# Kernel optimization log

Hardware: AMD Instinct MI355X
Metric: run time of the kernel (lower is better)

The kernel has to match this reference:

```python
import jax, jax.numpy as jnp
import numpy as np
import math

B, LAT, HID, T, NCLS = 128, 128, 256, 1920, 3
EPS = 1e-5


def _ln(x, g, b):
    m = jnp.mean(x, axis=-1, keepdims=True)
    v = jnp.var(x, axis=-1, keepdims=True)
    return (x - m) * jax.lax.rsqrt(v + EPS) * g + b


def _leaky(x):
    return jax.nn.leaky_relu(x, 0.2)


def _lstm_layer(x, Wih, Whh, bih, bhh):
    # x: [T, B, D] time-major; gate order i,f,g,o (PyTorch convention)
    xw = jnp.einsum('tbd,gd->tbg', x, Wih) + bih + bhh  # precompute input projection
    Hd = Whh.shape[1]
    bsz = x.shape[1]

    def step(carry, xg):
        h, c = carry
        gates = xg + h @ Whh.T
        i, f, g, o = jnp.split(gates, 4, axis=-1)
        c = jax.nn.sigmoid(f) * c + jax.nn.sigmoid(i) * jnp.tanh(g)
        h = jax.nn.sigmoid(o) * jnp.tanh(c)
        return (h, c), h

    init = (jnp.zeros((bsz, Hd), x.dtype), jnp.zeros((bsz, Hd), x.dtype))
    _, hs = jax.lax.scan(step, init, xw)
    return hs  # [T, B, H]


def setup_inputs() -> dict:
    key = jax.random.key(0)
    ks = jax.random.split(key, 16)
    s = 0.05
    H2 = HID // 2
    d = {
        'z': jax.random.normal(ks[0], (B, LAT), jnp.float32),
        'labels': jax.random.randint(ks[1], (B,), 0, 4, jnp.int64),
        'emb_W': jax.random.normal(ks[2], (NCLS + 1, HID), jnp.float32) * s,
        'np_W': jax.random.normal(ks[3], (HID, LAT + HID), jnp.float32) * s,
        'np_b': jnp.zeros((HID,), jnp.float32),
        'np_g': jnp.ones((HID,), jnp.float32),
        'np_be': jnp.zeros((HID,), jnp.float32),
        'Wih0': jax.random.normal(ks[4], (4 * HID, 2 * HID), jnp.float32) * s,
        'Whh0': jax.random.normal(ks[5], (4 * HID, HID), jnp.float32) * s,
        'bih0': jnp.zeros((4 * HID,), jnp.float32),
        'bhh0': jnp.zeros((4 * HID,), jnp.float32),
        'Wih1': jax.random.normal(ks[6], (4 * HID, HID), jnp.float32) * s,
        'Whh1': jax.random.normal(ks[7], (4 * HID, HID), jnp.float32) * s,
        'bih1': jnp.zeros((4 * HID,), jnp.float32),
        'bhh1': jnp.zeros((4 * HID,), jnp.float32),
        'oW1': jax.random.normal(ks[8], (H2, HID), jnp.float32) * s,
        'ob1': jnp.zeros((H2,), jnp.float32),
        'og': jnp.ones((H2,), jnp.float32),
        'obe': jnp.zeros((H2,), jnp.float32),
        'oW2': jax.random.normal(ks[9], (3, H2), jnp.float32) * s,
        'ob2': jnp.zeros((3,), jnp.float32),
        'sW1': jax.random.normal(ks[10], (H2, HID), jnp.float32) * s,
        'sb1': jnp.zeros((H2,), jnp.float32),
        'sg': jnp.ones((H2,), jnp.float32),
        'sbe': jnp.zeros((H2,), jnp.float32),
        'sW2': jax.random.normal(ks[11], (1, H2), jnp.float32) * s,
        'sb2': jnp.zeros((1,), jnp.float32),
        'stress_w': jnp.array(1.8, jnp.float32),
        'amu_w': jnp.array([0.15, 0.7, 0.15], jnp.float32),
        'amu_b': jnp.array(-0.3, jnp.float32),
    }
    return d


def reference(z, labels, emb_W, np_W, np_b, np_g, np_be, Wih0, Whh0, bih0, bhh0,
              Wih1, Whh1, bih1, bhh1, oW1, ob1, og, obe, oW2, ob2,
              sW1, sb1, sg, sbe, sW2, sb2, stress_w, amu_w, amu_b):
    bsz = z.shape[0]
    emb = emb_W[labels]                                   # [B, H]
    h = _leaky(_ln(jnp.concatenate([z, emb], axis=1) @ np_W.T + np_b, np_g, np_be))
    # [B, T, 2H]
    sig_in = jnp.concatenate([
        jnp.broadcast_to(h[:, None, :], (bsz, T, HID)),
        jnp.broadcast_to(emb[:, None, :], (bsz, T, HID)),
    ], axis=2)
    x = jnp.transpose(sig_in, (1, 0, 2))                  # time-major [T, B, 2H]
    x = _lstm_layer(x, Wih0, Whh0, bih0, bhh0)
    x = _lstm_layer(x, Wih1, Whh1, bih1, bhh1)
    ch = jnp.transpose(x, (1, 0, 2))                      # [B, T, H]

    # oscillation params per sample (vectorized over batch)
    h_avg = jnp.mean(ch, axis=1)                          # [B, H]
    op = _leaky(_ln(h_avg @ oW1.T + ob1, og, obe)) @ oW2.T + ob2  # [B, 3]
    freq = 0.23 + 0.04 * jnp.tanh(op[:, 0])
    amp = 2.0 + 1.5 * jnp.tanh(op[:, 1])
    phase = math.pi * jax.nn.sigmoid(op[:, 2])
    t = jnp.linspace(0.0, 1.0, T)
    osc = amp[:, None] * jnp.sin(2.0 * math.pi * freq[:, None] * T * t[None, :] + phase[:, None])  # [B, T]

    base = jnp.tanh(_leaky(_ln(ch @ sW1.T + sb1, sg, sbe)) @ sW2.T + sb2)  # [B, T, 1]
    enhanced = 0.6 * base[..., 0] + 0.4 * osc             # [B, T]

    stressed = stress_w * enhanced                        # conv1d k=1, w=1.8
    xp = jnp.pad(enhanced, ((0, 0), (1, 1)))
    smoothed = amu_w[0] * xp[:, :-2] + amu_w[1] * xp[:, 1:-1] + amu_w[2] * xp[:, 2:] + amu_b

    lab = labels[:, None]
    out = jnp.where(lab == 1, enhanced,
          jnp.where(lab == 2, stressed,
          jnp.where(lab == 3, smoothed, jnp.zeros_like(enhanced))))
    return out[..., None]                                  # [B, T, 1]
```

## Files before the change

### kernel.cpp

```cpp
#include <hip/hip_runtime.h>

#define TSTEPS 1920
#define NB 128
#define HIDN 256
#define LATN 128
#define EPSF 1e-5f

typedef __attribute__((ext_vector_type(8))) short bf16x8;
typedef __attribute__((ext_vector_type(4))) float f32x4;

__device__ __forceinline__ unsigned short f2bf(float x) {
    unsigned u = __builtin_bit_cast(unsigned, x);
    unsigned r = (u + 0x7fffu + ((u >> 16) & 1u)) >> 16;
    return (unsigned short)r;
}
__device__ __forceinline__ float bf2f(unsigned short h) {
    unsigned u = ((unsigned)h) << 16;
    return __builtin_bit_cast(float, u);
}
__device__ __forceinline__ float fsig(float x) {
    float e = __expf(-fabsf(x));
    float s = 1.f / (1.f + e);
    return x >= 0.f ? s : 1.f - s;
}
__device__ __forceinline__ float ftanh(float x) {
    float e = __expf(-2.f * fabsf(x));
    float r = (1.f - e) / (1.f + e);
    return x >= 0.f ? r : -r;
}
__device__ __forceinline__ float fleaky(float x) { return x > 0.f ? x : 0.2f * x; }
__device__ __forceinline__ bf16x8 bcast16(uint4 v) { return __builtin_bit_cast(bf16x8, v); }

__device__ __forceinline__ unsigned aload(const unsigned* p) {
    return __hip_atomic_load(p, __ATOMIC_RELAXED, __HIP_MEMORY_SCOPE_AGENT);
}
__device__ __forceinline__ unsigned long long aload64(const unsigned long long* p) {
    return __hip_atomic_load(p, __ATOMIC_RELAXED, __HIP_MEMORY_SCOPE_AGENT);
}
__device__ __forceinline__ void astore(unsigned* p, unsigned v) {
    __hip_atomic_store(p, v, __ATOMIC_RELAXED, __HIP_MEMORY_SCOPE_AGENT);
}

#define MFMA(a, b, c) __builtin_amdgcn_mfma_f32_16x16x32_bf16((a), (b), (c), 0, 0, 0)

#define FLG(g, s) ((g) * 8 + (s)) * 32
#define HPLANE(g, layer, buf) (((g) * 2 + (layer)) * 2 + (buf)) * 4096

__global__ void init_sync(unsigned* hbuf, unsigned* flags) {
    int i = blockIdx.x * 256 + threadIdx.x;
    if (i < 131072) hbuf[i] = 0u;
    if (i < 4096) flags[i] = 0u;
}

__global__ void pack_bfrag_sliced(const float* __restrict__ A, const float* __restrict__ Bsrc,
                                  int KA, int KB,
                                  unsigned short* __restrict__ hi, unsigned short* __restrict__ lo) {
    int e = blockIdx.x * 256 + threadIdx.x;
    int K = KA + KB;
    int KT = K >> 5;
    if (e >= 1024 * K) return;
    int j = e & 7;
    int l = (e >> 3) & 63;
    int r = e >> 9;
    int kt = r % KT;
    int r2 = r / KT;
    int v = r2 & 7;
    int w = r2 >> 3;
    int n = (v >> 1) * 256 + 32 * w + 16 * (v & 1) + (l & 15);
    int k = kt * 32 + (l >> 4) * 8 + j;
    float val = (k < KA) ? A[n * KA + k] : Bsrc[n * KB + (k - KA)];
    unsigned short h = f2bf(val);
    hi[e] = h;
    lo[e] = f2bf(val - bf2f(h));
}

__global__ void pack_sw1frag(const float* __restrict__ sW1, unsigned short* __restrict__ out) {
    int e = blockIdx.x * 256 + threadIdx.x;
    if (e >= 32768) return;
    int j3 = e & 7;
    int l = (e >> 3) & 63;
    int r = e >> 9;
    int kt = r & 7, w = r >> 3;
    int n = w * 16 + (l & 15);
    int k = kt * 32 + (l >> 4) * 8 + j3;
    out[e] = f2bf(sW1[n * 256 + k]);
}

__global__ void pack4T(const float* __restrict__ W, int N, int K, float* __restrict__ out) {
    int e = blockIdx.x * 256 + threadIdx.x;
    if (e >= N * K) return;
    int j = e & 3;
    int rest = e >> 2;
    int n = rest % N;
    int k4 = rest / N;
    out[e] = W[n * K + 4 * k4 + j];
}

__global__ void prep_b1(const float* __restrict__ bih1, const float* __restrict__ bhh1,
                        float* __restrict__ b1sum) {
    int i = blockIdx.x * 256 + threadIdx.x;
    if (i < 1024) b1sum[i] = bih1[i] + bhh1[i];
}

__global__ void np_head(const float* __restrict__ z, const int* __restrict__ labels,
                        const float* __restrict__ emb_W, const float* __restrict__ np_W,
                        const float* __restrict__ np_b, const float* __restrict__ np_g,
                        const float* __restrict__ np_be, float* __restrict__ x_const) {
    int b = blockIdx.x;
    int j = threadIdx.x;
    __shared__ float xc[LATN + HIDN];
    __shared__ float red[8];
    int lab = labels[b];
    if (j < LATN) xc[j] = z[b * LATN + j];
    float e = emb_W[lab * HIDN + j];
    xc[LATN + j] = e;
    __syncthreads();
    float d = np_b[j];
    for (int k = 0; k < LATN + HIDN; ++k) d += xc[k] * np_W[j * (LATN + HIDN) + k];
    int lane = j & 63, wv = j >> 6;
    float s = d, s2 = d * d;
    for (int o = 1; o < 64; o <<= 1) { s += __shfl_xor(s, o); s2 += __shfl_xor(s2, o); }
    if (lane == 0) { red[wv] = s; red[4 + wv] = s2; }
    __syncthreads();
    float S = red[0] + red[1] + red[2] + red[3];
    float S2 = red[4] + red[5] + red[6] + red[7];
    float m = S * (1.f / 256.f);
    float var = S2 * (1.f / 256.f) - m * m;
    float h = fleaky((d - m) * rsqrtf(var + EPSF) * np_g[j] + np_be[j]);
    x_const[b * 512 + j] = h;
    x_const[b * 512 + 256 + j] = e;
}

__global__ void __launch_bounds__(1024) xw0_kernel(const float* __restrict__ x_const,
                                                   const float4* __restrict__ Wih0T4,
                                                   const float* __restrict__ bih0,
                                                   const float* __restrict__ bhh0,
                                                   float* __restrict__ xw0) {
    int b = blockIdx.x;
    int g = threadIdx.x;
    __shared__ float xc[512];
    if (g < 512) xc[g] = x_const[b * 512 + g];
    __syncthreads();
    const float4* xc4 = (const float4*)xc;
    float4 acc = {0.f, 0.f, 0.f, 0.f};
#pragma unroll 8
    for (int k4 = 0; k4 < 128; ++k4) {
        float4 w = Wih0T4[k4 * 1024 + g];
        float4 x = xc4[k4];
        acc.x = fmaf(w.x, x.x, acc.x);
        acc.y = fmaf(w.y, x.y, acc.y);
        acc.z = fmaf(w.z, x.z, acc.z);
        acc.w = fmaf(w.w, x.w, acc.w);
    }
    xw0[b * 1024 + g] = bih0[g] + bhh0[g] + ((acc.x + acc.y) + (acc.z + acc.w));
}

__global__ void __launch_bounds__(512, 2) lstm_coop(
    const uint4* __restrict__ whh0h, const uint4* __restrict__ whh0l,
    const uint4* __restrict__ w1h, const uint4* __restrict__ w1l,
    const unsigned short* __restrict__ sw1f_g, const float* __restrict__ xw0g,
    const float* __restrict__ b1sum, const float* __restrict__ sb1,
    const float* __restrict__ sg, const float* __restrict__ sbe,
    const float* __restrict__ sW2, const float* __restrict__ sb2,
    unsigned* __restrict__ hbuf, unsigned* __restrict__ flags,
    float* __restrict__ base_out, float* __restrict__ hsum_out) {
    extern __shared__ char smem[];
    char* pHhi = smem;
    char* pHlo = smem + 16384;
    unsigned short* sw1f = (unsigned short*)(smem + 32768);
    float* gates0 = (float*)(smem + 98304);
    float* gates1 = (float*)(smem + 106752);
    float* s1b = (float*)(smem + 115200);

    const int gidx = blockIdx.x & 7;
    const int W = blockIdx.x >> 3;
    const int g16 = gidx * 16;
    const int tid = threadIdx.x;
    const int l = tid & 63;
    const int v = tid >> 6;
    const int ln16 = l & 15;
    const int kg = l >> 4;

    for (int i = tid; i < 16384; i += 512)
        ((unsigned*)sw1f)[i] = ((const unsigned*)sw1f_g)[i];

    uint4 b0h[8], b0l[8];
#pragma unroll
    for (int kt = 0; kt < 8; ++kt) {
        int idx = ((W * 8 + v) * 8 + kt) * 64 + l;
        b0h[kt] = whh0h[idx];
        b0l[kt] = whh0l[idx];
    }
    uint4 w1hR[16], w1lR[16];
#pragma unroll
    for (int kt = 0; kt < 16; ++kt) {
        int idx = ((W * 8 + v) * 16 + kt) * 64 + l;
        w1hR[kt] = w1h[idx];
        w1lR[kt] = w1l[idx];
    }

    const int row = tid >> 5;
    const int ul = tid & 31;
    const int ug = 32 * W + ul;
    float xwi[4], b1v[4];
#pragma unroll
    for (int gt = 0; gt < 4; ++gt) {
        xwi[gt] = xw0g[(g16 + row) * 1024 + gt * 256 + ug];
        b1v[gt] = b1sum[gt * 256 + ug];
    }
    float c0 = 0.f, c1 = 0.f, hs = 0.f;

    const float sb1a = sb1[2 * l], sb1b = sb1[2 * l + 1];
    const float sga = sg[2 * l], sgb = sg[2 * l + 1];
    const float sbea = sbe[2 * l], sbeb = sbe[2 * l + 1];
    const float sw2a = sW2[2 * l], sw2b = sW2[2 * l + 1];
    const float sb2v = sb2[0];

    unsigned* h0buf[2] = {hbuf + HPLANE(gidx, 0, 0), hbuf + HPLANE(gidx, 0, 1)};
    unsigned* h1buf[2] = {hbuf + HPLANE(gidx, 1, 0), hbuf + HPLANE(gidx, 1, 1)};
    unsigned* fl = flags + FLG(gidx, W);
    unsigned* flbase = flags + FLG(gidx, 0);

    const int abase = ln16 * 1024;
    const int aswz = (ln16 & 7) << 4;
    const int kgo = kg * 16;
    const int gcol = (v >> 1) * 32 + (v & 1) * 16 + ln16;

#define WAITF(tgtv)                                                              \
    {                                                                            \
        unsigned tgt = (unsigned)(tgtv);                                         \
        while (true) {                                                           \
            unsigned val = (l < 8) ? aload(flbase + l * 32) : tgt;               \
            if (__all((int)(val >= tgt))) break;                                 \
            __builtin_amdgcn_s_sleep(1);                                         \
        }                                                                        \
    }                                                                            \
    asm volatile("" ::: "memory");

#define STAGE2(src0, src1)                                                       \
    {                                                                            \
        const unsigned long long* sA = (const unsigned long long*)(src0);        \
        const unsigned long long* sB = (const unsigned long long*)(src1);        \
        _Pragma("unroll")                                                        \
        for (int it = 0; it < 4; ++it) {                                         \
            int i2 = tid + 512 * it;                                             \
            int r_ = i2 >> 7, u2 = i2 & 127;                                     \
            int swz = (r_ & 7) << 4;                                             \
            int off0 = r_ * 1024 + ((4 * u2) ^ swz);                             \
            unsigned long long vA = aload64(sA + r_ * 128 + u2);                 \
            unsigned a0 = (unsigned)vA, a1 = (unsigned)(vA >> 32);               \
            *(unsigned*)(pHhi + off0) = (a0 >> 16) | (a1 & 0xffff0000u);         \
            *(unsigned*)(pHlo + off0) = (a0 & 0xffffu) | (a1 << 16);             \
            int off1 = r_ * 1024 + ((512 + 4 * u2) ^ swz);                       \
            unsigned long long vB = aload64(sB + r_ * 128 + u2);                 \
            unsigned e0 = (unsigned)vB, e1 = (unsigned)(vB >> 32);               \
            *(unsigned*)(pHhi + off1) = (e0 >> 16) | (e1 & 0xffff0000u);         \
            *(unsigned*)(pHlo + off1) = (e0 & 0xffffu) | (e1 << 16);             \
        }                                                                        \
    }

#define HEADFIN(tout)                                                            \
    if (v < 4) {                                                                 \
        _Pragma("unroll")                                                        \
        for (int r4 = 0; r4 < 4; ++r4) {                                         \
            int hrw = v * 4 + r4;                                                \
            float2 sv = *(const float2*)&s1b[hrw * 132 + 2 * l];                 \
            float sA = sv.x + sb1a, sB = sv.y + sb1b;                            \
            float ssum = sA + sB, ssq = sA * sA + sB * sB;                       \
            _Pragma("unroll")                                                    \
            for (int o = 1; o < 64; o <<= 1) {                                   \
                ssum += __shfl_xor(ssum, o); ssq += __shfl_xor(ssq, o);          \
            }                                                                    \
            float m = ssum * (1.f / 128.f);                                      \
            float var = ssq * (1.f / 128.f) - m * m;                             \
            float rstd = rsqrtf(var + EPSF);                                     \
            float p0 = fleaky((sA - m) * rstd * sga + sbea);                     \
            float p1 = fleaky((sB - m) * rstd * sgb + sbeb);                     \
            float qd = p0 * sw2a + p1 * sw2b;                                    \
            _Pragma("unroll")                                                    \
            for (int o = 1; o < 64; o <<= 1) qd += __shfl_xor(qd, o);            \
            if (l == 0) base_out[(g16 + hrw) * TSTEPS + (tout)] = ftanh(qd + sb2v); \
        }                                                                        \
    }

    __syncthreads();

    for (int p = 0; p <= TSTEPS; ++p) {
        WAITF(p);
        STAGE2(h0buf[(p - 1) & 1], h1buf[p & 1]);
        __syncthreads();
        {
            f32x4 a0 = {0.f, 0.f, 0.f, 0.f};
            f32x4 a1 = {0.f, 0.f, 0.f, 0.f};
            f32x4 ah = {0.f, 0.f, 0.f, 0.f};
#pragma unroll
            for (int kt = 0; kt < 8; ++kt) {
                int aoff = abase + ((kt * 64 + kgo) ^ aswz);
                bf16x8 ahi = bcast16(*(const uint4*)(pHhi + aoff));
                bf16x8 alo = bcast16(*(const uint4*)(pHlo + aoff));
                bf16x8 bh = bcast16(b0h[kt]);
                bf16x8 bl = bcast16(b0l[kt]);
                a0 = MFMA(ahi, bh, a0); a0 = MFMA(alo, bh, a0); a0 = MFMA(ahi, bl, a0);
                bf16x8 ch = bcast16(w1hR[kt]);
                bf16x8 cl = bcast16(w1lR[kt]);
                a1 = MFMA(ahi, ch, a1); a1 = MFMA(alo, ch, a1); a1 = MFMA(ahi, cl, a1);
            }
#pragma unroll
            for (int kt = 8; kt < 16; ++kt) {
                int aoff = abase + ((kt * 64 + kgo) ^ aswz);
                bf16x8 ahi = bcast16(*(const uint4*)(pHhi + aoff));
                bf16x8 alo = bcast16(*(const uint4*)(pHlo + aoff));
                bf16x8 ch = bcast16(w1hR[kt]);
                bf16x8 cl = bcast16(w1lR[kt]);
                a1 = MFMA(ahi, ch, a1); a1 = MFMA(alo, ch, a1); a1 = MFMA(ahi, cl, a1);
                bf16x8 bsw = bcast16(*(const uint4*)&sw1f[((v * 8 + (kt - 8)) * 64 + l) * 8]);
                ah = MFMA(ahi, bsw, ah); ah = MFMA(alo, bsw, ah);
            }
#pragma unroll
            for (int r = 0; r < 4; ++r) {
                gates0[(kg * 4 + r) * 132 + gcol] = a0[r];
                gates1[(kg * 4 + r) * 132 + gcol] = a1[r];
                s1b[(kg * 4 + r) * 132 + v * 16 + ln16] = ah[r];
            }
        }
        __syncthreads();
        {
            float i_ = gates0[row * 132 + ul] + xwi[0];
            float f_ = gates0[row * 132 + 32 + ul] + xwi[1];
            float g_ = gates0[row * 132 + 64 + ul] + xwi[2];
            float o_ = gates0[row * 132 + 96 + ul] + xwi[3];
            c0 = fsig(f_) * c0 + fsig(i_) * ftanh(g_);
            float h = fsig(o_) * ftanh(c0);
            unsigned short hh = f2bf(h);
            unsigned short ll = f2bf(h - bf2f(hh));
            astore(h0buf[p & 1] + row * 256 + ug, ((unsigned)hh << 16) | (unsigned)ll);
        }
        if (p > 0) {
            float i_ = gates1[row * 132 + ul] + b1v[0];
            float f_ = gates1[row * 132 + 32 + ul] + b1v[1];
            float g_ = gates1[row * 132 + 64 + ul] + b1v[2];
            float o_ = gates1[row * 132 + 96 + ul] + b1v[3];
            c1 = fsig(f_) * c1 + fsig(i_) * ftanh(g_);
            float h = fsig(o_) * ftanh(c1);
            hs += h;
            unsigned short hh = f2bf(h);
            unsigned short ll = f2bf(h - bf2f(hh));
            astore(h1buf[(p - 1) & 1] + row * 256 + ug, ((unsigned)hh << 16) | (unsigned)ll);
        }
        asm volatile("s_waitcnt vmcnt(0)" ::: "memory");
        __syncthreads();
        if (tid == 0) astore(fl, (unsigned)(p + 1));
        if (p >= 2) HEADFIN(p - 2);
    }
    WAITF(TSTEPS + 1);
    STAGE2(h0buf[(TSTEPS + 1 - 1) & 1], h1buf[(TSTEPS + 1) & 1]);
    __syncthreads();
    {
        f32x4 ah = {0.f, 0.f, 0.f, 0.f};
#pragma unroll
        for (int kt = 8; kt < 16; ++kt) {
            int aoff = abase + ((kt * 64 + kgo) ^ aswz);
            bf16x8 ahi = bcast16(*(const uint4*)(pHhi + aoff));
            bf16x8 alo = bcast16(*(const uint4*)(pHlo + aoff));
            bf16x8 bsw = bcast16(*(const uint4*)&sw1f[((v * 8 + (kt - 8)) * 64 + l) * 8]);
            ah = MFMA(ahi, bsw, ah); ah = MFMA(alo, bsw, ah);
        }
#pragma unroll
        for (int r = 0; r < 4; ++r) s1b[(kg * 4 + r) * 132 + v * 16 + ln16] = ah[r];
    }
    __syncthreads();
    HEADFIN(TSTEPS - 1);
    hsum_out[(g16 + row) * HIDN + ug] = hs;
#undef WAITF
#undef STAGE2
#undef HEADFIN
}

__global__ void out_kernel(const float* __restrict__ hsum, const float* __restrict__ oW1,
                           const float* __restrict__ ob1, const float* __restrict__ og,
                           const float* __restrict__ obe, const float* __restrict__ oW2,
                           const float* __restrict__ ob2, const float* __restrict__ base,
                           const int* __restrict__ labels, const float* __restrict__ stress_w,
                           const float* __restrict__ amu_w, const float* __restrict__ amu_b,
                           float* __restrict__ out) {
    int b = blockIdx.x;
    int tid = threadIdx.x;
    int lane = tid & 63, wv = tid >> 6;
    __shared__ float havg[256];
    __shared__ float red[8];
    __shared__ float params[3];
    __shared__ float e_row[TSTEPS];
    havg[tid] = hsum[b * 256 + tid] * (1.f / (float)TSTEPS);
    __syncthreads();
    float d1 = 0.f;
    if (tid < 128) {
        d1 = ob1[tid];
        for (int k = 0; k < 256; ++k) d1 += havg[k] * oW1[tid * 256 + k];
    }
    float s = d1, s2 = d1 * d1;
    for (int o = 1; o < 64; o <<= 1) { s += __shfl_xor(s, o); s2 += __shfl_xor(s2, o); }
    if (lane == 0 && wv < 2) { red[wv] = s; red[2 + wv] = s2; }
    __syncthreads();
    float m = (red[0] + red[1]) * (1.f / 128.f);
    float var = (red[2] + red[3]) * (1.f / 128.f) - m * m;
    float rstd = rsqrtf(var + EPSF);
    float p = 0.f;
    if (tid < 128) p = fleaky((d1 - m) * rstd * og[tid] + obe[tid]);
    float q0 = tid < 128 ? p * oW2[0 * 128 + tid] : 0.f;
    float q1 = tid < 128 ? p * oW2[1 * 128 + tid] : 0.f;
    float q2 = tid < 128 ? p * oW2[2 * 128 + tid] : 0.f;
    for (int o = 1; o < 64; o <<= 1) {
        q0 += __shfl_xor(q0, o); q1 += __shfl_xor(q1, o); q2 += __shfl_xor(q2, o);
    }
    __syncthreads();
    if (lane == 0 && wv < 2) { red[wv] = q0; red[2 + wv] = q1; red[4 + wv] = q2; }
    __syncthreads();
    if (tid == 0) {
        float op0 = red[0] + red[1] + ob2[0];
        float op1 = red[2] + red[3] + ob2[1];
        float op2 = red[4] + red[5] + ob2[2];
        params[0] = 0.23f + 0.04f * ftanh(op0);
        params[1] = 2.0f + 1.5f * ftanh(op1);
        params[2] = 3.14159265358979f * fsig(op2);
    }
    __syncthreads();
    float freq = params[0], amp = params[1], ph = params[2];
    for (int t = tid; t < TSTEPS; t += 256) {
        float x = freq * ((float)TSTEPS * (float)t / (float)(TSTEPS - 1));
        x -= floorf(x);
        float osc = amp * __sinf(6.28318530717958647f * x + ph);
        e_row[t] = 0.6f * base[b * TSTEPS + t] + 0.4f * osc;
    }
    __syncthreads();
    int lab = labels[b];
    float sw = stress_w[0];
    float w0 = amu_w[0], w1 = amu_w[1], w2 = amu_w[2], ab = amu_b[0];
    for (int t = tid; t < TSTEPS; t += 256) {
        float e = e_row[t];
        float r;
        if (lab == 1) r = e;
        else if (lab == 2) r = sw * e;
        else if (lab == 3) {
            float em = t > 0 ? e_row[t - 1] : 0.f;
            float ep = t < TSTEPS - 1 ? e_row[t + 1] : 0.f;
            r = w0 * em + w1 * e + w2 * ep + ab;
        } else r = 0.f;
        out[b * TSTEPS + t] = r;
    }
}

extern "C" void kernel_launch(void* const* d_in, const int* in_sizes, int n_in,
                              void* d_out, int out_size, void* d_ws, size_t ws_size,
                              hipStream_t stream) {
    (void)in_sizes; (void)n_in; (void)out_size; (void)ws_size;
    const float* z      = (const float*)d_in[0];
    const int* labels   = (const int*)d_in[1];
    const float* emb_W  = (const float*)d_in[2];
    const float* np_W   = (const float*)d_in[3];
    const float* np_b   = (const float*)d_in[4];
    const float* np_g   = (const float*)d_in[5];
    const float* np_be  = (const float*)d_in[6];
    const float* Wih0   = (const float*)d_in[7];
    const float* Whh0   = (const float*)d_in[8];
    const float* bih0   = (const float*)d_in[9];
    const float* bhh0   = (const float*)d_in[10];
    const float* Wih1   = (const float*)d_in[11];
    const float* Whh1   = (const float*)d_in[12];
    const float* bih1   = (const float*)d_in[13];
    const float* bhh1   = (const float*)d_in[14];
    const float* oW1    = (const float*)d_in[15];
    const float* ob1    = (const float*)d_in[16];
    const float* og     = (const float*)d_in[17];
    const float* obe    = (const float*)d_in[18];
    const float* oW2    = (const float*)d_in[19];
    const float* ob2    = (const float*)d_in[20];
    const float* sW1    = (const float*)d_in[21];
    const float* sb1    = (const float*)d_in[22];
    const float* sg     = (const float*)d_in[23];
    const float* sbe    = (const float*)d_in[24];
    const float* sW2    = (const float*)d_in[25];
    const float* sb2    = (const float*)d_in[26];
    const float* stressw= (const float*)d_in[27];
    const float* amu_w  = (const float*)d_in[28];
    const float* amu_b  = (const float*)d_in[29];
    float* out = (float*)d_out;

    uint8_t* ws = (uint8_t*)d_ws;
    size_t off = 0;
    unsigned short* whh0h = (unsigned short*)(ws + off); off += (size_t)1024 * 256 * 2;
    unsigned short* whh0l = (unsigned short*)(ws + off); off += (size_t)1024 * 256 * 2;
    unsigned short* w1h   = (unsigned short*)(ws + off); off += (size_t)1024 * 512 * 2;
    unsigned short* w1l   = (unsigned short*)(ws + off); off += (size_t)1024 * 512 * 2;
    unsigned short* sw1fg = (unsigned short*)(ws + off); off += (size_t)32768 * 2;
    float* Wih0T4 = (float*)(ws + off); off += (size_t)1024 * 512 * 4;
    float* x_const= (float*)(ws + off); off += (size_t)NB * 512 * 4;
    float* xw0    = (float*)(ws + off); off += (size_t)NB * 1024 * 4;
    float* b1sum  = (float*)(ws + off); off += (size_t)1024 * 4;
    float* hsum   = (float*)(ws + off); off += (size_t)NB * 256 * 4;
    float* basef  = (float*)(ws + off); off += (size_t)NB * TSTEPS * 4;
    off = (off + 255) & ~(size_t)255;
    unsigned* hbuf = (unsigned*)(ws + off); off += (size_t)131072 * 4;
    unsigned* flags= (unsigned*)(ws + off); off += (size_t)4096 * 4;

    init_sync<<<512, 256, 0, stream>>>(hbuf, flags);
    pack_bfrag_sliced<<<1024, 256, 0, stream>>>(Whh0, nullptr, 256, 0, whh0h, whh0l);
    pack_bfrag_sliced<<<2048, 256, 0, stream>>>(Wih1, Whh1, 256, 256, w1h, w1l);
    pack_sw1frag<<<128, 256, 0, stream>>>(sW1, sw1fg);
    pack4T<<<2048, 256, 0, stream>>>(Wih0, 1024, 512, Wih0T4);
    prep_b1<<<4, 256, 0, stream>>>(bih1, bhh1, b1sum);

    np_head<<<NB, 256, 0, stream>>>(z, labels, emb_W, np_W, np_b, np_g, np_be, x_const);
    xw0_kernel<<<NB, 1024, 0, stream>>>(x_const, (const float4*)Wih0T4, bih0, bhh0, xw0);
    lstm_coop<<<64, 512, 123648, stream>>>((const uint4*)whh0h, (const uint4*)whh0l,
                                           (const uint4*)w1h, (const uint4*)w1l,
                                           sw1fg, xw0, b1sum, sb1, sg, sbe, sW2, sb2,
                                           hbuf, flags, basef, hsum);
    out_kernel<<<NB, 256, 0, stream>>>(hsum, oW1, ob1, og, obe, oW2, ob2, basef, labels,
                                       stressw, amu_w, amu_b, out);
}
```

Baseline: 27.60 ms.

## Split each batch group into two half-groups with interleaved independent recurrence phases

Each workgroup's 16-row batch slice is split into two independent 8-row sub-groups, each with its own h buffers, flags and LDS staging planes. Every timestep now runs two sub-phases back to back, so the cross-workgroup flag wait of one sub-group can overlap the compute of the other. The cost is twice as many wait/sync rounds per step, MFMAs that now carry only half the rows, more LDS (156KB), and more register pressure.

```diff
diff --git a/kernel.cpp b/kernel.cpp
--- a/kernel.cpp
+++ b/kernel.cpp
@@ -44,7 +44,7 @@
 #define MFMA(a, b, c) __builtin_amdgcn_mfma_f32_16x16x32_bf16((a), (b), (c), 0, 0, 0)
 
 #define FLG(g, s) ((g) * 8 + (s)) * 32
-#define HPLANE(g, layer, buf) (((g) * 2 + (layer)) * 2 + (buf)) * 4096
+#define HPLANE(g, layer, buf) ((((g) * 2 + (layer)) * 2 + (buf)) * 2048)
 
 __global__ void init_sync(unsigned* hbuf, unsigned* flags) {
     int i = blockIdx.x * 256 + threadIdx.x;
@@ -165,16 +165,17 @@
     unsigned* __restrict__ hbuf, unsigned* __restrict__ flags,
     float* __restrict__ base_out, float* __restrict__ hsum_out) {
     extern __shared__ char smem[];
-    char* pHhi = smem;
-    char* pHlo = smem + 16384;
-    unsigned short* sw1f = (unsigned short*)(smem + 32768);
-    float* gates0 = (float*)(smem + 98304);
-    float* gates1 = (float*)(smem + 106752);
-    float* s1b = (float*)(smem + 115200);
-
-    const int gidx = blockIdx.x & 7;
+    char* pAhi = smem;
+    char* pAlo = smem + 16384;
+    char* pBhi = smem + 32768;
+    char* pBlo = smem + 49152;
+    unsigned short* sw1f = (unsigned short*)(smem + 65536);
+    float* gates0 = (float*)(smem + 131072);
+    float* gates1 = (float*)(smem + 139520);
+    float* s1b    = (float*)(smem + 147968);
+
+    const int g8 = blockIdx.x & 7;
     const int W = blockIdx.x >> 3;
-    const int g16 = gidx * 16;
     const int tid = threadIdx.x;
     const int l = tid & 63;
     const int v = tid >> 6;
@@ -183,6 +184,10 @@
 
     for (int i = tid; i < 16384; i += 512)
         ((unsigned*)sw1f)[i] = ((const unsigned*)sw1f_g)[i];
+    for (int i = tid; i < 4096; i += 512) {
+        ((unsigned*)pAhi)[i] = 0u; ((unsigned*)pAlo)[i] = 0u;
+        ((unsigned*)pBhi)[i] = 0u; ((unsigned*)pBlo)[i] = 0u;
+    }
 
     uint4 b0h[8], b0l[8];
 #pragma unroll
@@ -199,16 +204,18 @@
         w1lR[kt] = w1l[idx];
     }
 
-    const int row = tid >> 5;
+    const int r8 = (tid >> 5) & 7;
     const int ul = tid & 31;
     const int ug = 32 * W + ul;
-    float xwi[4], b1v[4];
+    float xwiA[4], xwiB[4], b1v[4];
 #pragma unroll
     for (int gt = 0; gt < 4; ++gt) {
-        xwi[gt] = xw0g[(g16 + row) * 1024 + gt * 256 + ug];
+        xwiA[gt] = xw0g[(16 * g8 + r8) * 1024 + gt * 256 + ug];
+        xwiB[gt] = xw0g[(16 * g8 + 8 + r8) * 1024 + gt * 256 + ug];
         b1v[gt] = b1sum[gt * 256 + ug];
     }
-    float c0 = 0.f, c1 = 0.f, hs = 0.f;
+    float c0A = 0.f, c1A = 0.f, hsA = 0.f;
+    float c0B = 0.f, c1B = 0.f, hsB = 0.f;
 
     const float sb1a = sb1[2 * l], sb1b = sb1[2 * l + 1];
     const float sga = sg[2 * l], sgb = sg[2 * l + 1];
@@ -216,51 +223,128 @@
     const float sw2a = sW2[2 * l], sw2b = sW2[2 * l + 1];
     const float sb2v = sb2[0];
 
-    unsigned* h0buf[2] = {hbuf + HPLANE(gidx, 0, 0), hbuf + HPLANE(gidx, 0, 1)};
-    unsigned* h1buf[2] = {hbuf + HPLANE(gidx, 1, 0), hbuf + HPLANE(gidx, 1, 1)};
-    unsigned* fl = flags + FLG(gidx, W);
-    unsigned* flbase = flags + FLG(gidx, 0);
+    unsigned* h0A[2] = {hbuf + HPLANE(2 * g8, 0, 0), hbuf + HPLANE(2 * g8, 0, 1)};
+    unsigned* h1A[2] = {hbuf + HPLANE(2 * g8, 1, 0), hbuf + HPLANE(2 * g8, 1, 1)};
+    unsigned* h0B[2] = {hbuf + HPLANE(2 * g8 + 1, 0, 0), hbuf + HPLANE(2 * g8 + 1, 0, 1)};
+    unsigned* h1B[2] = {hbuf + HPLANE(2 * g8 + 1, 1, 0), hbuf + HPLANE(2 * g8 + 1, 1, 1)};
+    unsigned* flA = flags + FLG(2 * g8, W);
+    unsigned* flAb = flags + FLG(2 * g8, 0);
+    unsigned* flB = flags + FLG(2 * g8 + 1, W);
+    unsigned* flBb = flags + FLG(2 * g8 + 1, 0);
 
     const int abase = ln16 * 1024;
     const int aswz = (ln16 & 7) << 4;
     const int kgo = kg * 16;
     const int gcol = (v >> 1) * 32 + (v & 1) * 16 + ln16;
 
-#define WAITF(tgtv)                                                              \
+#define WAITF(BASE, tgtv)                                                        \
     {                                                                            \
         unsigned tgt = (unsigned)(tgtv);                                         \
         while (true) {                                                           \
-            unsigned val = (l < 8) ? aload(flbase + l * 32) : tgt;               \
+            unsigned val = (l < 8) ? aload((BASE) + l * 32) : tgt;               \
             if (__all((int)(val >= tgt))) break;                                 \
             __builtin_amdgcn_s_sleep(1);                                         \
         }                                                                        \
     }                                                                            \
     asm volatile("" ::: "memory");
 
-#define STAGE2(src0, src1)                                                       \
+#define STAGE2(DH, DL, SRC0, SRC1)                                               \
     {                                                                            \
-        const unsigned long long* sA = (const unsigned long long*)(src0);        \
-        const unsigned long long* sB = (const unsigned long long*)(src1);        \
+        const unsigned long long* sA_ = (const unsigned long long*)(SRC0);       \
+        const unsigned long long* sB_ = (const unsigned long long*)(SRC1);       \
         _Pragma("unroll")                                                        \
         for (int it = 0; it < 4; ++it) {                                         \
             int i2 = tid + 512 * it;                                             \
-            int r_ = i2 >> 7, u2 = i2 & 127;                                     \
-            int swz = (r_ & 7) << 4;                                             \
-            int off0 = r_ * 1024 + ((4 * u2) ^ swz);                             \
-            unsigned long long vA = aload64(sA + r_ * 128 + u2);                 \
-            unsigned a0 = (unsigned)vA, a1 = (unsigned)(vA >> 32);               \
-            *(unsigned*)(pHhi + off0) = (a0 >> 16) | (a1 & 0xffff0000u);         \
-            *(unsigned*)(pHlo + off0) = (a0 & 0xffffu) | (a1 << 16);             \
-            int off1 = r_ * 1024 + ((512 + 4 * u2) ^ swz);                       \
-            unsigned long long vB = aload64(sB + r_ * 128 + u2);                 \
-            unsigned e0 = (unsigned)vB, e1 = (unsigned)(vB >> 32);               \
-            *(unsigned*)(pHhi + off1) = (e0 >> 16) | (e1 & 0xffff0000u);         \
-            *(unsigned*)(pHlo + off1) = (e0 & 0xffffu) | (e1 << 16);             \
-        }                                                                        \
-    }
-
-#define HEADFIN(tout)                                                            \
-    if (v < 4) {                                                                 \
+            int rr = i2 >> 7, u2 = i2 & 127;                                     \
+            int prow = rr & 7;                                                   \
+            int bas = (rr >> 3) * 512;                                           \
+            const unsigned long long* sp = (rr < 8) ? sA_ : sB_;                 \
+            unsigned long long vv = aload64(sp + prow * 128 + u2);               \
+            unsigned w0_ = (unsigned)vv, w1_ = (unsigned)(vv >> 32);             \
+            int off = prow * 1024 + ((bas + 4 * u2) ^ (prow << 4));              \
+            *(unsigned*)((DH) + off) = (w0_ >> 16) | (w1_ & 0xffff0000u);        \
+            *(unsigned*)((DL) + off) = (w0_ & 0xffffu) | (w1_ << 16);            \
+        }                                                                        \
+    }
+
+#define MVPHASE(PH, PL)                                                          \
+    {                                                                            \
+        f32x4 a0 = {0.f, 0.f, 0.f, 0.f};                                         \
+        f32x4 a1 = {0.f, 0.f, 0.f, 0.f};                                         \
+        f32x4 ahd = {0.f, 0.f, 0.f, 0.f};                                        \
+        _Pragma("unroll")                                                        \
+        for (int kt = 0; kt < 8; ++kt) {                                         \
+            int aoff = abase + ((kt * 64 + kgo) ^ aswz);                         \
+            bf16x8 ahi = bcast16(*(const uint4*)((PH) + aoff));                  \
+            bf16x8 alo = bcast16(*(const uint4*)((PL) + aoff));                  \
+            bf16x8 bh = bcast16(b0h[kt]);                                        \
+            bf16x8 bl = bcast16(b0l[kt]);                                        \
+            a0 = MFMA(ahi, bh, a0); a0 = MFMA(alo, bh, a0); a0 = MFMA(ahi, bl, a0); \
+            bf16x8 ch = bcast16(w1hR[kt]);                                       \
+            bf16x8 cl = bcast16(w1lR[kt]);                                       \
+            a1 = MFMA(ahi, ch, a1); a1 = MFMA(alo, ch, a1); a1 = MFMA(ahi, cl, a1); \
+        }                                                                        \
+        _Pragma("unroll")                                                        \
+        for (int kt = 8; kt < 16; ++kt) {                                        \
+            int aoff = abase + ((kt * 64 + kgo) ^ aswz);                         \
+            bf16x8 ahi = bcast16(*(const uint4*)((PH) + aoff));                  \
+            bf16x8 alo = bcast16(*(const uint4*)((PL) + aoff));                  \
+            bf16x8 ch = bcast16(w1hR[kt]);                                       \
+            bf16x8 cl = bcast16(w1lR[kt]);                                       \
+            a1 = MFMA(ahi, ch, a1); a1 = MFMA(alo, ch, a1); a1 = MFMA(ahi, cl, a1); \
+            bf16x8 bsw = bcast16(*(const uint4*)&sw1f[((v * 8 + (kt - 8)) * 64 + l) * 8]); \
+            ahd = MFMA(ahi, bsw, ahd); ahd = MFMA(alo, bsw, ahd);                \
+        }                                                                        \
+        _Pragma("unroll")                                                        \
+        for (int r = 0; r < 4; ++r) {                                            \
+            gates0[(kg * 4 + r) * 132 + gcol] = a0[r];                           \
+            gates1[(kg * 4 + r) * 132 + gcol] = a1[r];                           \
+            s1b[(kg * 4 + r) * 132 + v * 16 + ln16] = ahd[r];                    \
+        }                                                                        \
+    }
+
+#define HEADMV(PH, PL)                                                           \
+    {                                                                            \
+        f32x4 ahd = {0.f, 0.f, 0.f, 0.f};                                        \
+        _Pragma("unroll")                                                        \
+        for (int kt = 8; kt < 16; ++kt) {                                        \
+            int aoff = abase + ((kt * 64 + kgo) ^ aswz);                         \
+            bf16x8 ahi = bcast16(*(const uint4*)((PH) + aoff));                  \
+            bf16x8 alo = bcast16(*(const uint4*)((PL) + aoff));                  \
+            bf16x8 bsw = bcast16(*(const uint4*)&sw1f[((v * 8 + (kt - 8)) * 64 + l) * 8]); \
+            ahd = MFMA(ahi, bsw, ahd); ahd = MFMA(alo, bsw, ahd);                \
+        }                                                                        \
+        _Pragma("unroll")                                                        \
+        for (int r = 0; r < 4; ++r) s1b[(kg * 4 + r) * 132 + v * 16 + ln16] = ahd[r]; \
+    }
+
+#define UPDPUB(pp, H0B, H1B, XWI, C0, C1, HS)                                    \
+    if (tid < 256) {                                                             \
+        float i_ = gates0[r8 * 132 + ul] + (XWI)[0];                             \
+        float f_ = gates0[r8 * 132 + 32 + ul] + (XWI)[1];                        \
+        float g_ = gates0[r8 * 132 + 64 + ul] + (XWI)[2];                        \
+        float o_ = gates0[r8 * 132 + 96 + ul] + (XWI)[3];                        \
+        C0 = fsig(f_) * C0 + fsig(i_) * ftanh(g_);                               \
+        float h = fsig(o_) * ftanh(C0);                                          \
+        unsigned short hh = f2bf(h);                                             \
+        unsigned short ll = f2bf(h - bf2f(hh));                                  \
+        astore((H0B)[(pp) & 1] + r8 * 256 + ug, ((unsigned)hh << 16) | (unsigned)ll); \
+        if ((pp) > 0) {                                                          \
+            i_ = gates1[r8 * 132 + ul] + b1v[0];                                 \
+            f_ = gates1[r8 * 132 + 32 + ul] + b1v[1];                            \
+            g_ = gates1[r8 * 132 + 64 + ul] + b1v[2];                            \
+            o_ = gates1[r8 * 132 + 96 + ul] + b1v[3];                            \
+            C1 = fsig(f_) * C1 + fsig(i_) * ftanh(g_);                           \
+            h = fsig(o_) * ftanh(C1);                                            \
+            HS += h;                                                             \
+            hh = f2bf(h);                                                        \
+            ll = f2bf(h - bf2f(hh));                                             \
+            astore((H1B)[((pp) - 1) & 1] + r8 * 256 + ug, ((unsigned)hh << 16) | (unsigned)ll); \
+        }                                                                        \
+    }
+
+#define HEADFIN(GROW, tout)                                                      \
+    if (v < 2) {                                                                 \
         _Pragma("unroll")                                                        \
         for (int r4 = 0; r4 < 4; ++r4) {                                         \
             int hrw = v * 4 + r4;                                                \
@@ -279,101 +363,53 @@
             float qd = p0 * sw2a + p1 * sw2b;                                    \
             _Pragma("unroll")                                                    \
             for (int o = 1; o < 64; o <<= 1) qd += __shfl_xor(qd, o);            \
-            if (l == 0) base_out[(g16 + hrw) * TSTEPS + (tout)] = ftanh(qd + sb2v); \
-        }                                                                        \
-    }
+            if (l == 0) base_out[((GROW) + hrw) * TSTEPS + (tout)] = ftanh(qd + sb2v); \
+        }                                                                        \
+    }
+
+#define SUBPHASE(pp, PH, PL, H0B, H1B, FLW, FLWB, XWI, C0, C1, HS, GROW)         \
+    WAITF(FLWB, pp);                                                             \
+    STAGE2(PH, PL, (H0B)[((pp) - 1) & 1], (H1B)[(pp) & 1]);                      \
+    __syncthreads();                                                             \
+    MVPHASE(PH, PL);                                                             \
+    __syncthreads();                                                             \
+    UPDPUB(pp, H0B, H1B, XWI, C0, C1, HS);                                       \
+    asm volatile("s_waitcnt vmcnt(0)" ::: "memory");                             \
+    __syncthreads();                                                             \
+    if (tid == 0) astore(FLW, (unsigned)((pp) + 1));                             \
+    if ((pp) >= 2) HEADFIN(GROW, (pp) - 2);
 
     __syncthreads();
 
     for (int p = 0; p <= TSTEPS; ++p) {
-        WAITF(p);
-        STAGE2(h0buf[(p - 1) & 1], h1buf[p & 1]);
-        __syncthreads();
-        {
-            f32x4 a0 = {0.f, 0.f, 0.f, 0.f};
-            f32x4 a1 = {0.f, 0.f, 0.f, 0.f};
-            f32x4 ah = {0.f, 0.f, 0.f, 0.f};
-#pragma unroll
-            for (int kt = 0; kt < 8; ++kt) {
-                int aoff = abase + ((kt * 64 + kgo) ^ aswz);
-                bf16x8 ahi = bcast16(*(const uint4*)(pHhi + aoff));
-                bf16x8 alo = bcast16(*(const uint4*)(pHlo + aoff));
-                bf16x8 bh = bcast16(b0h[kt]);
-                bf16x8 bl = bcast16(b0l[kt]);
-                a0 = MFMA(ahi, bh, a0); a0 = MFMA(alo, bh, a0); a0 = MFMA(ahi, bl, a0);
-                bf16x8 ch = bcast16(w1hR[kt]);
-                bf16x8 cl = bcast16(w1lR[kt]);
-                a1 = MFMA(ahi, ch, a1); a1 = MFMA(alo, ch, a1); a1 = MFMA(ahi, cl, a1);
-            }
-#pragma unroll
-            for (int kt = 8; kt < 16; ++kt) {
-                int aoff = abase + ((kt * 64 + kgo) ^ aswz);
-                bf16x8 ahi = bcast16(*(const uint4*)(pHhi + aoff));
-                bf16x8 alo = bcast16(*(const uint4*)(pHlo + aoff));
-                bf16x8 ch = bcast16(w1hR[kt]);
-                bf16x8 cl = bcast16(w1lR[kt]);
-                a1 = MFMA(ahi, ch, a1); a1 = MFMA(alo, ch, a1); a1 = MFMA(ahi, cl, a1);
-                bf16x8 bsw = bcast16(*(const uint4*)&sw1f[((v * 8 + (kt - 8)) * 64 + l) * 8]);
-                ah = MFMA(ahi, bsw, ah); ah = MFMA(alo, bsw, ah);
-            }
-#pragma unroll
-            for (int r = 0; r < 4; ++r) {
-                gates0[(kg * 4 + r) * 132 + gcol] = a0[r];
-                gates1[(kg * 4 + r) * 132 + gcol] = a1[r];
-                s1b[(kg * 4 + r) * 132 + v * 16 + ln16] = ah[r];
-            }
-        }
-        __syncthreads();
-        {
-            float i_ = gates0[row * 132 + ul] + xwi[0];
-            float f_ = gates0[row * 132 + 32 + ul] + xwi[1];
-            float g_ = gates0[row * 132 + 64 + ul] + xwi[2];
-            float o_ = gates0[row * 132 + 96 + ul] + xwi[3];
-            c0 = fsig(f_) * c0 + fsig(i_) * ftanh(g_);
-            float h = fsig(o_) * ftanh(c0);
-            unsigned short hh = f2bf(h);
-            unsigned short ll = f2bf(h - bf2f(hh));
-            astore(h0buf[p & 1] + row * 256 + ug, ((unsigned)hh << 16) | (unsigned)ll);
-        }
-        if (p > 0) {
-            float i_ = gates1[row * 132 + ul] + b1v[0];
-            float f_ = gates1[row * 132 + 32 + ul] + b1v[1];
-            float g_ = gates1[row * 132 + 64 + ul] + b1v[2];
-            float o_ = gates1[row * 132 + 96 + ul] + b1v[3];
-            c1 = fsig(f_) * c1 + fsig(i_) * ftanh(g_);
-            float h = fsig(o_) * ftanh(c1);
-            hs += h;
-            unsigned short hh = f2bf(h);
-            unsigned short ll = f2bf(h - bf2f(hh));
-            astore(h1buf[(p - 1) & 1] + row * 256 + ug, ((unsigned)hh << 16) | (unsigned)ll);
-        }
-        asm volatile("s_waitcnt vmcnt(0)" ::: "memory");
-        __syncthreads();
-        if (tid == 0) astore(fl, (unsigned)(p + 1));
-        if (p >= 2) HEADFIN(p - 2);
-    }
-    WAITF(TSTEPS + 1);
-    STAGE2(h0buf[(TSTEPS + 1 - 1) & 1], h1buf[(TSTEPS + 1) & 1]);
-    __syncthreads();
-    {
-        f32x4 ah = {0.f, 0.f, 0.f, 0.f};
-#pragma unroll
-        for (int kt = 8; kt < 16; ++kt) {
-            int aoff = abase + ((kt * 64 + kgo) ^ aswz);
-            bf16x8 ahi = bcast16(*(const uint4*)(pHhi + aoff));
-            bf16x8 alo = bcast16(*(const uint4*)(pHlo + aoff));
-            bf16x8 bsw = bcast16(*(const uint4*)&sw1f[((v * 8 + (kt - 8)) * 64 + l) * 8]);
-            ah = MFMA(ahi, bsw, ah); ah = MFMA(alo, bsw, ah);
-        }
-#pragma unroll
-        for (int r = 0; r < 4; ++r) s1b[(kg * 4 + r) * 132 + v * 16 + ln16] = ah[r];
-    }
-    __syncthreads();
-    HEADFIN(TSTEPS - 1);
-    hsum_out[(g16 + row) * HIDN + ug] = hs;
+        SUBPHASE(p, pAhi, pAlo, h0A, h1A, flA, flAb, xwiA, c0A, c1A, hsA, 16 * g8);
+        SUBPHASE(p, pBhi, pBlo, h0B, h1B, flB, flBb, xwiB, c0B, c1B, hsB, 16 * g8 + 8);
+    }
+
+    WAITF(flAb, TSTEPS + 1);
+    STAGE2(pAhi, pAlo, h0A[(TSTEPS - 1) & 1], h1A[(TSTEPS - 1) & 1]);
+    __syncthreads();
+    HEADMV(pAhi, pAlo);
+    __syncthreads();
+    HEADFIN(16 * g8, TSTEPS - 1);
+    __syncthreads();
+    WAITF(flBb, TSTEPS + 1);
+    STAGE2(pBhi, pBlo, h0B[(TSTEPS - 1) & 1], h1B[(TSTEPS - 1) & 1]);
+    __syncthreads();
+    HEADMV(pBhi, pBlo);
+    __syncthreads();
+    HEADFIN(16 * g8 + 8, TSTEPS - 1);
+    if (tid < 256) {
+        hsum_out[(16 * g8 + r8) * HIDN + ug] = hsA;
+        hsum_out[(16 * g8 + 8 + r8) * HIDN + ug] = hsB;
+    }
 #undef WAITF
 #undef STAGE2
+#undef MVPHASE
+#undef HEADMV
+#undef UPDPUB
 #undef HEADFIN
+#undef SUBPHASE
 }
 
 __global__ void out_kernel(const float* __restrict__ hsum, const float* __restrict__ oW1,
@@ -511,7 +547,7 @@
 
     np_head<<<NB, 256, 0, stream>>>(z, labels, emb_W, np_W, np_b, np_g, np_be, x_const);
     xw0_kernel<<<NB, 1024, 0, stream>>>(x_const, (const float4*)Wih0T4, bih0, bhh0, xw0);
-    lstm_coop<<<64, 512, 123648, stream>>>((const uint4*)whh0h, (const uint4*)whh0l,
+    lstm_coop<<<64, 512, 156416, stream>>>((const uint4*)whh0h, (const uint4*)whh0l,
                                            (const uint4*)w1h, (const uint4*)w1l,
                                            sw1fg, xw0, b1sum, sb1, sg, sbe, sW2, sb2,
                                            hbuf, flags, basef, hsum);
```

Result: slower. 42.39 ms (+53.6%).
